# Optimization experiments

Hardware: AMD Instinct MI355X
Metric: run time of the kernel (lower is better)

## Reference

```python
import jax, jax.numpy as jnp
import numpy as np

B = 262144
VD = 64          # vector_dim
N_ACTION = 8     # n_orientation + n_position
N_TYPE = 5
IN_DIM = 6 + N_ACTION  # (n_orientation + n_bounding_box) + n_action = 14


def _linear_init(k, fan_in, fan_out):
    k1, k2 = jax.random.split(k)
    s = 1.0 / np.sqrt(fan_in)
    W = jax.random.uniform(k1, (fan_in, fan_out), minval=-s, maxval=s, dtype=jnp.float32)
    b = jax.random.uniform(k2, (fan_out,), minval=-s, maxval=s, dtype=jnp.float32)
    return W, b


def setup_inputs() -> dict:
    key = jax.random.key(0)
    ks = jax.random.split(key, 12)
    W1, b1 = _linear_init(ks[0], IN_DIM, VD)
    W1b, b1b = _linear_init(ks[1], VD, VD)
    W1c, b1c = _linear_init(ks[2], VD, VD)
    W2a, b2a = _linear_init(ks[3], VD, N_ACTION)
    W2b, b2b = _linear_init(ks[4], VD, 1)
    Ta1, ta1 = _linear_init(ks[5], N_TYPE, VD)
    Ta2, ta2 = _linear_init(ks[6], VD, VD)
    Tb1, tb1 = _linear_init(ks[7], N_TYPE, VD)
    Tb2, tb2 = _linear_init(ks[8], VD, VD)
    states = jax.random.normal(ks[9], (B, 3, 18), dtype=jnp.float32)
    action = jax.random.normal(ks[10], (B, N_ACTION), dtype=jnp.float32)
    b_type = jax.random.normal(ks[11], (B, N_TYPE), dtype=jnp.float32)
    table = jnp.zeros((B, 6), dtype=jnp.float32)
    return dict(states=states, action=action, b_type=b_type, table=table,
                W1=W1, b1=b1, W1b=W1b, b1b=b1b, W1c=W1c, b1c=b1c,
                W2a=W2a, b2a=b2a, W2b=W2b, b2b=b2b,
                Ta1=Ta1, ta1=ta1, Ta2=Ta2, ta2=ta2,
                Tb1=Tb1, tb1=tb1, Tb2=Tb2, tb2=tb2)


def reference(states, action, b_type, table,
              W1, b1, W1b, b1b, W1c, b1c, W2a, b2a, W2b, b2b,
              Ta1, ta1, Ta2, ta2, Tb1, tb1, Tb2, tb2):
    def type_mlp(t, Wx, bx, Wy, by):  # Linear -> Tanh -> Linear -> Tanh
        return jnp.tanh(jnp.tanh(t @ Wx + bx) @ Wy + by)

    gate1 = type_mlp(b_type, Ta1, ta1, Ta2, ta2)  # [B, VD], type_a(b_type)

    # relative_positions: repeat action over n_blocks+1 slots, subtract block xy from first 3
    rel = jnp.tile(action[:, None, :], (1, 4, 1))          # [B, 4, 8]
    rel = rel.at[:, :3, :2].add(-states[:, :, :2])

    types = states[..., 13:18]                             # [B, 3, 5]
    st = states[..., 3:9]                                  # orientation+bbox slice, [B, 3, 6]

    def stack(x, g1):  # tanh(l1) -> tanh(l1b) -> *type_1 -> tanh(l1c)
        h = jnp.tanh(x @ W1 + b1)
        h = jnp.tanh(h @ W1b + b1b) * g1
        return jnp.tanh(h @ W1c + b1c)

    # table branch (no second type gating)
    h_t = stack(jnp.concatenate([rel[:, 3], table], axis=-1), gate1)  # [B, VD]
    w_t = jax.nn.sigmoid(h_t @ W2b + b2b)                             # [B, 1]
    v_t = h_t @ W2a + b2a                                             # [B, 8]

    # three neighbor branches, vectorized over the block axis
    xin = jnp.concatenate([rel[:, :3], st], axis=-1)       # [B, 3, 14]
    h = stack(xin, gate1[:, None, :])                      # [B, 3, VD]
    h = h * type_mlp(types, Tb1, tb1, Tb2, tb2)            # gate by type_b(types[:, i])
    w = jax.nn.sigmoid(h @ W2b + b2b)                      # [B, 3, 1]
    v = h @ W2a + b2a                                      # [B, 3, 8]

    mask = st[:, :, 0:1] != -1.0                           # [B, 3, 1]
    w = jnp.where(mask, w, 0.0)

    residuals = w_t * v_t + jnp.sum(w * v, axis=1)         # [B, 8]
    return residuals + action
```

## Files before the change

### kernel.cpp

```cpp
#include <hip/hip_runtime.h>

typedef unsigned int  uint;
typedef unsigned short u16;
typedef __attribute__((ext_vector_type(8))) short bf16x8;
typedef __attribute__((ext_vector_type(4))) float f32x4;

#define OF_W1B   0
#define OF_W1C   4096
#define OF_TA2   8192
#define OF_TB2   12288
#define SHW_U16  16384
#define OF_W1    16384
#define OF_TA1   18432
#define OF_TB1   20480
#define OF_W2AB  22528
#define WTOT     23552
#define BTA2 0
#define BTB2 64
#define BB1B 128
#define BB1C 192
#define BH   256
#define BIASN 272

#if defined(__has_builtin) && __has_builtin(__builtin_amdgcn_exp2f)
#define EXP2F(x) __builtin_amdgcn_exp2f(x)
#else
#define EXP2F(x) __expf((x) * 0.6931471805599453f)
#endif
#if defined(__has_builtin) && __has_builtin(__builtin_amdgcn_rcpf)
#define RCPF(x) __builtin_amdgcn_rcpf(x)
#else
#define RCPF(x) __fdividef(1.0f, (x))
#endif

__device__ __forceinline__ float ftanh(float x){
    const float e = EXP2F(x * 2.8853900817779268f);
    return __builtin_fmaf(-2.0f, RCPF(e + 1.0f), 1.0f);
}
__device__ __forceinline__ float fsigm(float x){
    return RCPF(1.0f + EXP2F(-1.4426950408889634f * x));
}
__device__ __forceinline__ uint cvtpk(float lo, float hi){
    uint r; asm("v_cvt_pk_bf16_f32 %0, %1, %2" : "=v"(r) : "v"(lo), "v"(hi)); return r;
}
__device__ __forceinline__ u16 bfb(float x){
    union { float f; uint u; } v; v.f = x;
    return (u16)((v.u + 0x7fffu + ((v.u >> 16) & 1u)) >> 16);
}
__device__ __forceinline__ f32x4 MFMA(bf16x8 a, bf16x8 b, f32x4 c){
    return __builtin_amdgcn_mfma_f32_16x16x32_bf16(a, b, c, 0, 0, 0);
}

__device__ __forceinline__ void zacc(f32x4 (&acc)[4][2]){
    #pragma unroll
    for (int mt = 0; mt < 4; ++mt)
        #pragma unroll
        for (int n = 0; n < 2; ++n) acc[mt][n] = f32x4{0.f, 0.f, 0.f, 0.f};
}
__device__ __forceinline__ void ld_bias(const float* SB, int bb, int q, f32x4 (&acc)[4][2]){
    #pragma unroll
    for (int mt = 0; mt < 4; ++mt){
        const f32x4 b4 = *(const f32x4*)&SB[bb + 16*mt + 4*q];
        acc[mt][0] = b4; acc[mt][1] = b4;
    }
}

__device__ __forceinline__ void layer_k32(const u16* __restrict__ AbG, const u16* Bb, int WB,
                                          f32x4 (&acc)[4][2]){
    bf16x8 A[4];
    #pragma unroll
    for (int mt = 0; mt < 4; ++mt) A[mt] = *(const bf16x8*)&AbG[WB + mt*512];
    #pragma unroll
    for (int n = 0; n < 2; ++n){
        const bf16x8 B = *(const bf16x8*)&Bb[n*1024];
        #pragma unroll
        for (int mt = 0; mt < 4; ++mt) acc[mt][n] = MFMA(A[mt], B, acc[mt][n]);
    }
}
__device__ __forceinline__ void layer_k64(const u16* AbL, const u16* Bb, int WB,
                                          f32x4 (&acc)[4][2]){
    #pragma unroll
    for (int s = 0; s < 2; ++s){
        bf16x8 A[4];
        #pragma unroll
        for (int mt = 0; mt < 4; ++mt) A[mt] = *(const bf16x8*)&AbL[WB + (mt*2+s)*512];
        #pragma unroll
        for (int n = 0; n < 2; ++n){
            const bf16x8 B = *(const bf16x8*)&Bb[n*1024 + s*512];
            #pragma unroll
            for (int mt = 0; mt < 4; ++mt) acc[mt][n] = MFMA(A[mt], B, acc[mt][n]);
        }
    }
}
__device__ __forceinline__ void head_k64(const u16* __restrict__ AbG, const u16* Bb,
                                         f32x4 (&ah)[2]){
    const bf16x8 A0 = *(const bf16x8*)&AbG[OF_W2AB];
    const bf16x8 A1 = *(const bf16x8*)&AbG[OF_W2AB + 512];
    #pragma unroll
    for (int n = 0; n < 2; ++n){
        const bf16x8 B0 = *(const bf16x8*)&Bb[n*1024];
        const bf16x8 B1 = *(const bf16x8*)&Bb[n*1024 + 512];
        ah[n] = MFMA(A0, B0, ah[n]);
        ah[n] = MFMA(A1, B1, ah[n]);
    }
}

__device__ __forceinline__ void stD(u16* EW, int mt, int n, uint lo, uint hi){
    *(uint2*)&EW[(n*2 + (mt>>1))*512 + (mt&1)*256] = make_uint2(lo, hi);
}
__device__ __forceinline__ void epi_tanh(u16* EW, const f32x4 (&acc)[4][2]){
    #pragma unroll
    for (int mt = 0; mt < 4; ++mt)
        #pragma unroll
        for (int n = 0; n < 2; ++n)
            stD(EW, mt, n, cvtpk(ftanh(acc[mt][n][0]), ftanh(acc[mt][n][1])),
                           cvtpk(ftanh(acc[mt][n][2]), ftanh(acc[mt][n][3])));
}

template<int NR>
__device__ __forceinline__ void write_xrow(u16* ACW, int lane, const float (&x)[NR]){
    uint buf[16];
    #pragma unroll
    for (int i = 0; i < 16; ++i){
        if (2*i < NR){
            const float lo = x[2*i];
            const float hi = (2*i+1 < NR) ? x[2*i+1] : 0.f;
            buf[i] = cvtpk(lo, hi);
        } else buf[i] = 0u;
    }
    buf[15] = 0x3F800000u;
    const int c = lane & 31, n = c >> 4, col = c & 15, h = lane >> 5;
    #pragma unroll
    for (int gg = 0; gg < 2; ++gg){
        const int g = 2*h + gg;
        *(uint4*)&ACW[n*1024 + (g*16 + col)*8] =
            make_uint4(buf[4*g], buf[4*g+1], buf[4*g+2], buf[4*g+3]);
    }
}

__global__ __launch_bounds__(256)
void prep_weights(const float* __restrict__ W1,  const float* __restrict__ b1,
                  const float* __restrict__ W1b, const float* __restrict__ b1b,
                  const float* __restrict__ W1c, const float* __restrict__ b1c,
                  const float* __restrict__ W2a, const float* __restrict__ b2a,
                  const float* __restrict__ W2b, const float* __restrict__ b2b,
                  const float* __restrict__ Ta1, const float* __restrict__ ta1,
                  const float* __restrict__ Ta2, const float* __restrict__ ta2,
                  const float* __restrict__ Tb1, const float* __restrict__ tb1,
                  const float* __restrict__ Tb2, const float* __restrict__ tb2,
                  u16* __restrict__ WS)
{
    const int b = blockIdx.x, tid = threadIdx.x;
    if (b < 4){
        const float* Wg = (b==0) ? W1b : (b==1) ? W1c : (b==2) ? Ta2 : Tb2;
        const int    bb = (b==0) ? OF_W1B : (b==1) ? OF_W1C : (b==2) ? OF_TA2 : OF_TB2;
        #pragma unroll 1
        for (int idx = tid; idx < 4096; idx += 256){
            const int k = idx >> 6, j = idx & 63;
            WS[bb + (((j>>4)<<1)|(k>>5))*512 + ((j&15)|(((k>>3)&3)<<4))*8 + (k&7)] = bfb(Wg[idx]);
        }
        return;
    }
    float* WB = (float*)(WS + WTOT);
    #pragma unroll 1
    for (int i = tid; i < (WTOT - OF_W1); i += 256) WS[OF_W1 + i] = 0;
    __syncthreads();
    #pragma unroll 1
    for (int idx = tid; idx < 896; idx += 256){
        const int k = idx >> 6, j = idx & 63;
        WS[OF_W1 + (j>>4)*512 + ((j&15)|(((k>>3)&3)<<4))*8 + (k&7)] = bfb(W1[idx]);
    }
    #pragma unroll 1
    for (int idx = tid; idx < 320; idx += 256){
        const int k = idx >> 6, j = idx & 63;
        const int d = (j>>4)*512 + ((j&15)|(((k>>3)&3)<<4))*8 + (k&7);
        WS[OF_TA1 + d] = bfb(Ta1[idx]);
        WS[OF_TB1 + d] = bfb(Tb1[idx]);
    }
    #pragma unroll 1
    for (int idx = tid; idx < 512; idx += 256){
        const int j = idx >> 3, i = idx & 7;
        WS[OF_W2AB + (j>>5)*512 + (i|(((j>>3)&3)<<4))*8 + (j&7)] = bfb(W2a[idx]);
    }
    if (tid < 64){
        const int j = tid;
        WS[OF_W2AB + (j>>5)*512 + (8|(((j>>3)&3)<<4))*8 + (j&7)] = bfb(W2b[j]);
        const int d31 = ((j&15)|(3<<4))*8 + 7;
        WS[OF_W1  + (j>>4)*512 + d31] = bfb(b1[j]);
        WS[OF_TA1 + (j>>4)*512 + d31] = bfb(ta1[j]);
        WS[OF_TB1 + (j>>4)*512 + d31] = bfb(tb1[j]);
        WB[BTA2+j] = ta2[j]; WB[BTB2+j] = tb2[j];
        WB[BB1B+j] = b1b[j]; WB[BB1C+j] = b1c[j];
    }
    if (tid < 16) WB[BH+tid] = (tid < 8) ? b2a[tid] : (tid == 8 ? b2b[0] : 0.0f);
}

__global__ __launch_bounds__(256)
__attribute__((amdgpu_waves_per_eu(3, 3)))
void net_mfma(const float* __restrict__ states, const float* __restrict__ action,
              const float* __restrict__ b_type, const float* __restrict__ table,
              const u16* __restrict__ WS, int Btot, float* __restrict__ out)
{
    __shared__ u16   SHW[SHW_U16];
    __shared__ float SBIAS[BIASN];
    __shared__ u16   ACT[4*2048];

    const int tid  = threadIdx.x;
    const int lane = tid & 63;
    const int q    = lane >> 4;
    const int wv   = tid >> 6;

    {
        const uint4* src = (const uint4*)WS;
        uint4* dst = (uint4*)SHW;
        #pragma unroll 1
        for (int i = tid; i < SHW_U16/8; i += 256) dst[i] = src[i];
        const float* bg = (const float*)(WS + WTOT);
        #pragma unroll 1
        for (int i = tid; i < BIASN; i += 256) SBIAS[i] = bg[i];
    }
    __syncthreads();

    u16* ACW = &ACT[wv << 11];
    const u16* AbG = &WS[lane*8];
    const u16* AbL = &SHW[lane*8];
    const u16* Bb  = &ACW[lane*8];
    u16* EW = &ACW[(q>>1)*128 + (lane&15)*8 + 4*(q&1)];

    const int ebw   = blockIdx.x*128 + wv*32;
    const int elast = Btot - 1;
    const int eme   = min(ebw + (lane & 31), elast);

    float a8[8];
    { const float* ap = action + (size_t)eme*8;
      const float4 a0 = *(const float4*)ap; const float4 a1 = *(const float4*)(ap+4);
      a8[0]=a0.x; a8[1]=a0.y; a8[2]=a0.z; a8[3]=a0.w; a8[4]=a1.x; a8[5]=a1.y; a8[6]=a1.z; a8[7]=a1.w; }
    const float* sp = states + (size_t)eme*54;

    uint2 gp[4][2];
    {
        float x5[5];
        { const float* bp = b_type + (size_t)eme*5;
          #pragma unroll
          for (int k = 0; k < 5; ++k) x5[k] = bp[k]; }
        write_xrow<5>(ACW, lane, x5);
        f32x4 acc[4][2];
        zacc(acc);
        layer_k32(AbG, Bb, OF_TA1, acc);
        epi_tanh(EW, acc);
        ld_bias(SBIAS, BTA2, q, acc);
        layer_k64(AbL, Bb, OF_TA2, acc);
        #pragma unroll
        for (int mt = 0; mt < 4; ++mt)
            #pragma unroll
            for (int n = 0; n < 2; ++n)
                gp[mt][n] = make_uint2(cvtpk(ftanh(acc[mt][n][0]), ftanh(acc[mt][n][1])),
                                       cvtpk(ftanh(acc[mt][n][2]), ftanh(acc[mt][n][3])));
    }

    f32x4 ro[2];
    ro[0] = f32x4{0.f,0.f,0.f,0.f}; ro[1] = f32x4{0.f,0.f,0.f,0.f};

    #pragma unroll 1
    for (int r = 0; r < 4; ++r){
        const bool ht = (r < 3);
        uint2 tgp[4][2];
        f32x4 acc[4][2];

        if (ht){
            float xt[5];
            #pragma unroll
            for (int k = 0; k < 5; ++k) xt[k] = sp[r*18 + 13 + k];
            write_xrow<5>(ACW, lane, xt);
            zacc(acc);
            layer_k32(AbG, Bb, OF_TB1, acc);
            epi_tanh(EW, acc);
            ld_bias(SBIAS, BTB2, q, acc);
            layer_k64(AbL, Bb, OF_TB2, acc);
            #pragma unroll
            for (int mt = 0; mt < 4; ++mt)
                #pragma unroll
                for (int n = 0; n < 2; ++n)
                    tgp[mt][n] = make_uint2(cvtpk(ftanh(acc[mt][n][0]), ftanh(acc[mt][n][1])),
                                            cvtpk(ftanh(acc[mt][n][2]), ftanh(acc[mt][n][3])));
        }

        float x14[14]; float maskf = 1.0f;
        #pragma unroll
        for (int k = 0; k < 8; ++k) x14[k] = a8[k];
        if (ht){
            x14[0] -= sp[r*18 + 0];
            x14[1] -= sp[r*18 + 1];
            #pragma unroll
            for (int k = 0; k < 6; ++k) x14[8 + k] = sp[r*18 + 3 + k];
            maskf = (x14[8] == -1.0f) ? 0.0f : 1.0f;
        } else {
            const float* tp = table + (size_t)eme*6;
            #pragma unroll
            for (int k = 0; k < 6; ++k) x14[8 + k] = tp[k];
        }
        write_xrow<14>(ACW, lane, x14);

        zacc(acc);
        layer_k32(AbG, Bb, OF_W1, acc);
        epi_tanh(EW, acc);

        ld_bias(SBIAS, BB1B, q, acc);
        layer_k64(AbL, Bb, OF_W1B, acc);
        #pragma unroll
        for (int mt = 0; mt < 4; ++mt)
            #pragma unroll
            for (int n = 0; n < 2; ++n){
                const uint lo = gp[mt][n].x, hi = gp[mt][n].y;
                const float t0 = ftanh(acc[mt][n][0]) * __uint_as_float(lo << 16);
                const float t1 = ftanh(acc[mt][n][1]) * __uint_as_float(lo & 0xffff0000u);
                const float t2 = ftanh(acc[mt][n][2]) * __uint_as_float(hi << 16);
                const float t3 = ftanh(acc[mt][n][3]) * __uint_as_float(hi & 0xffff0000u);
                stD(EW, mt, n, cvtpk(t0, t1), cvtpk(t2, t3));
            }

        ld_bias(SBIAS, BB1C, q, acc);
        layer_k64(AbL, Bb, OF_W1C, acc);
        #pragma unroll
        for (int mt = 0; mt < 4; ++mt)
            #pragma unroll
            for (int n = 0; n < 2; ++n){
                float m0 = 1.f, m1 = 1.f, m2 = 1.f, m3 = 1.f;
                if (ht){
                    const uint lo = tgp[mt][n].x, hi = tgp[mt][n].y;
                    m0 = __uint_as_float(lo << 16); m1 = __uint_as_float(lo & 0xffff0000u);
                    m2 = __uint_as_float(hi << 16); m3 = __uint_as_float(hi & 0xffff0000u);
                }
                stD(EW, mt, n, cvtpk(ftanh(acc[mt][n][0])*m0, ftanh(acc[mt][n][1])*m1),
                               cvtpk(ftanh(acc[mt][n][2])*m2, ftanh(acc[mt][n][3])*m3));
            }

        f32x4 ah[2];
        { const f32x4 b4 = *(const f32x4*)&SBIAS[BH + 4*q];
          ah[0] = b4; ah[1] = b4; }
        head_k64(AbG, Bb, ah);

        #pragma unroll
        for (int n = 0; n < 2; ++n){
            const float wm = fsigm(ah[n][0]);
            const float w  = __shfl(wm, 32 + (lane & 15), 64)
                           * __shfl(maskf, 16*n + (lane & 15), 64);
            #pragma unroll
            for (int c = 0; c < 4; ++c) ro[n][c] += w * ah[n][c];
        }
    }

    if (lane < 32){
        #pragma unroll
        for (int n = 0; n < 2; ++n){
            const int e2 = ebw + 16*n + (lane & 15);
            if (e2 < Btot){
                const int co = 4*q;
                const float4 av = *(const float4*)(action + (size_t)e2*8 + co);
                float4 res;
                res.x = av.x + ro[n][0]; res.y = av.y + ro[n][1];
                res.z = av.z + ro[n][2]; res.w = av.w + ro[n][3];
                *(float4*)(out + (size_t)e2*8 + co) = res;
            }
        }
    }
}

extern "C" void kernel_launch(void* const* d_in, const int* in_sizes, int n_in,
                              void* d_out, int out_size, void* d_ws, size_t ws_size,
                              hipStream_t stream)
{
    const float* states = (const float*)d_in[0];
    const float* action = (const float*)d_in[1];
    const float* b_type = (const float*)d_in[2];
    const float* table  = (const float*)d_in[3];
    const float* W1  = (const float*)d_in[4];
    const float* b1  = (const float*)d_in[5];
    const float* W1b = (const float*)d_in[6];
    const float* b1b = (const float*)d_in[7];
    const float* W1c = (const float*)d_in[8];
    const float* b1c = (const float*)d_in[9];
    const float* W2a = (const float*)d_in[10];
    const float* b2a = (const float*)d_in[11];
    const float* W2b = (const float*)d_in[12];
    const float* b2b = (const float*)d_in[13];
    const float* Ta1 = (const float*)d_in[14];
    const float* ta1 = (const float*)d_in[15];
    const float* Ta2 = (const float*)d_in[16];
    const float* ta2 = (const float*)d_in[17];
    const float* Tb1 = (const float*)d_in[18];
    const float* tb1 = (const float*)d_in[19];
    const float* Tb2 = (const float*)d_in[20];
    const float* tb2 = (const float*)d_in[21];
    float* out = (float*)d_out;
    u16* WS = (u16*)d_ws;

    const int Btot = in_sizes[1] / 8;
    prep_weights<<<dim3(5), dim3(256), 0, stream>>>(
        W1, b1, W1b, b1b, W1c, b1c, W2a, b2a, W2b, b2b,
        Ta1, ta1, Ta2, ta2, Tb1, tb1, Tb2, tb2, WS);
    const int grid = (Btot + 127) / 128;
    net_mfma<<<dim3(grid), dim3(256), 0, stream>>>(
        states, action, b_type, table, WS, Btot, out);
}
```

Measured before the change: 142.9 us.

## Split MFMA layers per N-tile and double block size to raise occupancy

Each layer now runs over the two 16-column N tiles one at a time, with sched_barrier fences between them, so only four accumulator tiles are live at once instead of eight. Weight A-fragments are loaded inside the MFMA loop rather than preloaded. The block grows to 512 threads (8 waves, 256 elements) with waves_per_eu relaxed to 3-4, so the shared-memory weight copy is amortised over more elements and occupancy can rise. The cost is repeated A-fragment loads for each N tile, and the fences limit how much the compiler can overlap MFMA with the tanh epilogue.

```diff
diff --git a/kernel.cpp b/kernel.cpp
--- a/kernel.cpp
+++ b/kernel.cpp
@@ -32,6 +32,7 @@
 #else
 #define RCPF(x) __fdividef(1.0f, (x))
 #endif
+#define SCHED_FENCE() __builtin_amdgcn_sched_barrier(0)
 
 __device__ __forceinline__ float ftanh(float x){
     const float e = EXP2F(x * 2.8853900817779268f);
@@ -51,70 +52,56 @@
     return __builtin_amdgcn_mfma_f32_16x16x32_bf16(a, b, c, 0, 0, 0);
 }
 
-__device__ __forceinline__ void zacc(f32x4 (&acc)[4][2]){
+__device__ __forceinline__ void zacc4(f32x4 (&acc)[4]){
+    #pragma unroll
+    for (int mt = 0; mt < 4; ++mt) acc[mt] = f32x4{0.f, 0.f, 0.f, 0.f};
+}
+__device__ __forceinline__ void ldb4(const float* SB, int bb, int q, f32x4 (&acc)[4]){
     #pragma unroll
     for (int mt = 0; mt < 4; ++mt)
-        #pragma unroll
-        for (int n = 0; n < 2; ++n) acc[mt][n] = f32x4{0.f, 0.f, 0.f, 0.f};
-}
-__device__ __forceinline__ void ld_bias(const float* SB, int bb, int q, f32x4 (&acc)[4][2]){
+        acc[mt] = *(const f32x4*)&SB[bb + 16*mt + 4*q];
+}
+
+__device__ __forceinline__ void k32_n(const u16* __restrict__ Ab, const u16* Bb, int WB,
+                                      int n, f32x4 (&acc)[4]){
+    const bf16x8 B = *(const bf16x8*)&Bb[n*1024];
     #pragma unroll
     for (int mt = 0; mt < 4; ++mt){
-        const f32x4 b4 = *(const f32x4*)&SB[bb + 16*mt + 4*q];
-        acc[mt][0] = b4; acc[mt][1] = b4;
-    }
-}
-
-__device__ __forceinline__ void layer_k32(const u16* __restrict__ AbG, const u16* Bb, int WB,
-                                          f32x4 (&acc)[4][2]){
-    bf16x8 A[4];
-    #pragma unroll
-    for (int mt = 0; mt < 4; ++mt) A[mt] = *(const bf16x8*)&AbG[WB + mt*512];
-    #pragma unroll
-    for (int n = 0; n < 2; ++n){
-        const bf16x8 B = *(const bf16x8*)&Bb[n*1024];
-        #pragma unroll
-        for (int mt = 0; mt < 4; ++mt) acc[mt][n] = MFMA(A[mt], B, acc[mt][n]);
-    }
-}
-__device__ __forceinline__ void layer_k64(const u16* AbL, const u16* Bb, int WB,
-                                          f32x4 (&acc)[4][2]){
+        const bf16x8 A = *(const bf16x8*)&Ab[WB + mt*512];
+        acc[mt] = MFMA(A, B, acc[mt]);
+    }
+}
+__device__ __forceinline__ void k64_n(const u16* AbL, const u16* Bb, int WB,
+                                      int n, f32x4 (&acc)[4]){
     #pragma unroll
     for (int s = 0; s < 2; ++s){
-        bf16x8 A[4];
-        #pragma unroll
-        for (int mt = 0; mt < 4; ++mt) A[mt] = *(const bf16x8*)&AbL[WB + (mt*2+s)*512];
-        #pragma unroll
-        for (int n = 0; n < 2; ++n){
-            const bf16x8 B = *(const bf16x8*)&Bb[n*1024 + s*512];
-            #pragma unroll
-            for (int mt = 0; mt < 4; ++mt) acc[mt][n] = MFMA(A[mt], B, acc[mt][n]);
-        }
-    }
-}
-__device__ __forceinline__ void head_k64(const u16* __restrict__ AbG, const u16* Bb,
-                                         f32x4 (&ah)[2]){
-    const bf16x8 A0 = *(const bf16x8*)&AbG[OF_W2AB];
-    const bf16x8 A1 = *(const bf16x8*)&AbG[OF_W2AB + 512];
-    #pragma unroll
-    for (int n = 0; n < 2; ++n){
-        const bf16x8 B0 = *(const bf16x8*)&Bb[n*1024];
-        const bf16x8 B1 = *(const bf16x8*)&Bb[n*1024 + 512];
-        ah[n] = MFMA(A0, B0, ah[n]);
-        ah[n] = MFMA(A1, B1, ah[n]);
-    }
+        const bf16x8 B = *(const bf16x8*)&Bb[n*1024 + s*512];
+        #pragma unroll
+        for (int mt = 0; mt < 4; ++mt){
+            const bf16x8 A = *(const bf16x8*)&AbL[WB + (mt*2+s)*512];
+            acc[mt] = MFMA(A, B, acc[mt]);
+        }
+    }
+}
+__device__ __forceinline__ f32x4 head_n(const u16* __restrict__ Ab, const u16* Bb,
+                                        int n, f32x4 ah){
+    #pragma unroll
+    for (int s = 0; s < 2; ++s){
+        const bf16x8 A = *(const bf16x8*)&Ab[OF_W2AB + s*512];
+        const bf16x8 B = *(const bf16x8*)&Bb[n*1024 + s*512];
+        ah = MFMA(A, B, ah);
+    }
+    return ah;
 }
 
 __device__ __forceinline__ void stD(u16* EW, int mt, int n, uint lo, uint hi){
     *(uint2*)&EW[(n*2 + (mt>>1))*512 + (mt&1)*256] = make_uint2(lo, hi);
 }
-__device__ __forceinline__ void epi_tanh(u16* EW, const f32x4 (&acc)[4][2]){
+__device__ __forceinline__ void epi_tanh_n(u16* EW, int n, const f32x4 (&acc)[4]){
     #pragma unroll
     for (int mt = 0; mt < 4; ++mt)
-        #pragma unroll
-        for (int n = 0; n < 2; ++n)
-            stD(EW, mt, n, cvtpk(ftanh(acc[mt][n][0]), ftanh(acc[mt][n][1])),
-                           cvtpk(ftanh(acc[mt][n][2]), ftanh(acc[mt][n][3])));
+        stD(EW, mt, n, cvtpk(ftanh(acc[mt][0]), ftanh(acc[mt][1])),
+                       cvtpk(ftanh(acc[mt][2]), ftanh(acc[mt][3])));
 }
 
 template<int NR>
@@ -195,15 +182,15 @@
     if (tid < 16) WB[BH+tid] = (tid < 8) ? b2a[tid] : (tid == 8 ? b2b[0] : 0.0f);
 }
 
-__global__ __launch_bounds__(256)
-__attribute__((amdgpu_waves_per_eu(3, 3)))
+__global__ __launch_bounds__(512)
+__attribute__((amdgpu_waves_per_eu(3, 4)))
 void net_mfma(const float* __restrict__ states, const float* __restrict__ action,
               const float* __restrict__ b_type, const float* __restrict__ table,
               const u16* __restrict__ WS, int Btot, float* __restrict__ out)
 {
     __shared__ u16   SHW[SHW_U16];
     __shared__ float SBIAS[BIASN];
-    __shared__ u16   ACT[4*2048];
+    __shared__ u16   ACT[8*2048];
 
     const int tid  = threadIdx.x;
     const int lane = tid & 63;
@@ -214,10 +201,9 @@
         const uint4* src = (const uint4*)WS;
         uint4* dst = (uint4*)SHW;
         #pragma unroll 1
-        for (int i = tid; i < SHW_U16/8; i += 256) dst[i] = src[i];
+        for (int i = tid; i < SHW_U16/8; i += 512) dst[i] = src[i];
         const float* bg = (const float*)(WS + WTOT);
-        #pragma unroll 1
-        for (int i = tid; i < BIASN; i += 256) SBIAS[i] = bg[i];
+        if (tid < BIASN) SBIAS[tid] = bg[tid];
     }
     __syncthreads();
 
@@ -227,7 +213,7 @@
     const u16* Bb  = &ACW[lane*8];
     u16* EW = &ACW[(q>>1)*128 + (lane&15)*8 + 4*(q&1)];
 
-    const int ebw   = blockIdx.x*128 + wv*32;
+    const int ebw   = blockIdx.x*256 + wv*32;
     const int elast = Btot - 1;
     const int eme   = min(ebw + (lane & 31), elast);
 
@@ -244,18 +230,20 @@
           #pragma unroll
           for (int k = 0; k < 5; ++k) x5[k] = bp[k]; }
         write_xrow<5>(ACW, lane, x5);
-        f32x4 acc[4][2];
-        zacc(acc);
-        layer_k32(AbG, Bb, OF_TA1, acc);
-        epi_tanh(EW, acc);
-        ld_bias(SBIAS, BTA2, q, acc);
-        layer_k64(AbL, Bb, OF_TA2, acc);
-        #pragma unroll
-        for (int mt = 0; mt < 4; ++mt)
-            #pragma unroll
-            for (int n = 0; n < 2; ++n)
-                gp[mt][n] = make_uint2(cvtpk(ftanh(acc[mt][n][0]), ftanh(acc[mt][n][1])),
-                                       cvtpk(ftanh(acc[mt][n][2]), ftanh(acc[mt][n][3])));
+        #pragma unroll
+        for (int n = 0; n < 2; ++n){
+            f32x4 acc[4];
+            zacc4(acc);
+            k32_n(AbG, Bb, OF_TA1, n, acc);
+            epi_tanh_n(EW, n, acc);
+            ldb4(SBIAS, BTA2, q, acc);
+            k64_n(AbL, Bb, OF_TA2, n, acc);
+            #pragma unroll
+            for (int mt = 0; mt < 4; ++mt)
+                gp[mt][n] = make_uint2(cvtpk(ftanh(acc[mt][0]), ftanh(acc[mt][1])),
+                                       cvtpk(ftanh(acc[mt][2]), ftanh(acc[mt][3])));
+            SCHED_FENCE();
+        }
     }
 
     f32x4 ro[2];
@@ -265,24 +253,26 @@
     for (int r = 0; r < 4; ++r){
         const bool ht = (r < 3);
         uint2 tgp[4][2];
-        f32x4 acc[4][2];
 
         if (ht){
             float xt[5];
             #pragma unroll
             for (int k = 0; k < 5; ++k) xt[k] = sp[r*18 + 13 + k];
             write_xrow<5>(ACW, lane, xt);
-            zacc(acc);
-            layer_k32(AbG, Bb, OF_TB1, acc);
-            epi_tanh(EW, acc);
-            ld_bias(SBIAS, BTB2, q, acc);
-            layer_k64(AbL, Bb, OF_TB2, acc);
-            #pragma unroll
-            for (int mt = 0; mt < 4; ++mt)
+            #pragma unroll
+            for (int n = 0; n < 2; ++n){
+                f32x4 acc[4];
+                zacc4(acc);
+                k32_n(AbG, Bb, OF_TB1, n, acc);
+                epi_tanh_n(EW, n, acc);
+                ldb4(SBIAS, BTB2, q, acc);
+                k64_n(AbL, Bb, OF_TB2, n, acc);
                 #pragma unroll
-                for (int n = 0; n < 2; ++n)
-                    tgp[mt][n] = make_uint2(cvtpk(ftanh(acc[mt][n][0]), ftanh(acc[mt][n][1])),
-                                            cvtpk(ftanh(acc[mt][n][2]), ftanh(acc[mt][n][3])));
+                for (int mt = 0; mt < 4; ++mt)
+                    tgp[mt][n] = make_uint2(cvtpk(ftanh(acc[mt][0]), ftanh(acc[mt][1])),
+                                            cvtpk(ftanh(acc[mt][2]), ftanh(acc[mt][3])));
+                SCHED_FENCE();
+            }
         }
 
         float x14[14]; float maskf = 1.0f;
@@ -301,52 +291,61 @@
         }
         write_xrow<14>(ACW, lane, x14);
 
-        zacc(acc);
-        layer_k32(AbG, Bb, OF_W1, acc);
-        epi_tanh(EW, acc);
-
-        ld_bias(SBIAS, BB1B, q, acc);
-        layer_k64(AbL, Bb, OF_W1B, acc);
-        #pragma unroll
-        for (int mt = 0; mt < 4; ++mt)
-            #pragma unroll
-            for (int n = 0; n < 2; ++n){
+        #pragma unroll
+        for (int n = 0; n < 2; ++n){
+            f32x4 acc[4];
+            zacc4(acc);
+            k32_n(AbG, Bb, OF_W1, n, acc);
+            epi_tanh_n(EW, n, acc);
+            SCHED_FENCE();
+        }
+
+        #pragma unroll
+        for (int n = 0; n < 2; ++n){
+            f32x4 acc[4];
+            ldb4(SBIAS, BB1B, q, acc);
+            k64_n(AbL, Bb, OF_W1B, n, acc);
+            #pragma unroll
+            for (int mt = 0; mt < 4; ++mt){
                 const uint lo = gp[mt][n].x, hi = gp[mt][n].y;
-                const float t0 = ftanh(acc[mt][n][0]) * __uint_as_float(lo << 16);
-                const float t1 = ftanh(acc[mt][n][1]) * __uint_as_float(lo & 0xffff0000u);
-                const float t2 = ftanh(acc[mt][n][2]) * __uint_as_float(hi << 16);
-                const float t3 = ftanh(acc[mt][n][3]) * __uint_as_float(hi & 0xffff0000u);
+                const float t0 = ftanh(acc[mt][0]) * __uint_as_float(lo << 16);
+                const float t1 = ftanh(acc[mt][1]) * __uint_as_float(lo & 0xffff0000u);
+                const float t2 = ftanh(acc[mt][2]) * __uint_as_float(hi << 16);
+                const float t3 = ftanh(acc[mt][3]) * __uint_as_float(hi & 0xffff0000u);
                 stD(EW, mt, n, cvtpk(t0, t1), cvtpk(t2, t3));
             }
-
-        ld_bias(SBIAS, BB1C, q, acc);
-        layer_k64(AbL, Bb, OF_W1C, acc);
-        #pragma unroll
-        for (int mt = 0; mt < 4; ++mt)
-            #pragma unroll
-            for (int n = 0; n < 2; ++n){
+            SCHED_FENCE();
+        }
+
+        #pragma unroll
+        for (int n = 0; n < 2; ++n){
+            f32x4 acc[4];
+            ldb4(SBIAS, BB1C, q, acc);
+            k64_n(AbL, Bb, OF_W1C, n, acc);
+            #pragma unroll
+            for (int mt = 0; mt < 4; ++mt){
                 float m0 = 1.f, m1 = 1.f, m2 = 1.f, m3 = 1.f;
                 if (ht){
                     const uint lo = tgp[mt][n].x, hi = tgp[mt][n].y;
                     m0 = __uint_as_float(lo << 16); m1 = __uint_as_float(lo & 0xffff0000u);
                     m2 = __uint_as_float(hi << 16); m3 = __uint_as_float(hi & 0xffff0000u);
                 }
-                stD(EW, mt, n, cvtpk(ftanh(acc[mt][n][0])*m0, ftanh(acc[mt][n][1])*m1),
-                               cvtpk(ftanh(acc[mt][n][2])*m2, ftanh(acc[mt][n][3])*m3));
+                stD(EW, mt, n, cvtpk(ftanh(acc[mt][0])*m0, ftanh(acc[mt][1])*m1),
+                               cvtpk(ftanh(acc[mt][2])*m2, ftanh(acc[mt][3])*m3));
             }
-
-        f32x4 ah[2];
-        { const f32x4 b4 = *(const f32x4*)&SBIAS[BH + 4*q];
-          ah[0] = b4; ah[1] = b4; }
-        head_k64(AbG, Bb, ah);
-
-        #pragma unroll
-        for (int n = 0; n < 2; ++n){
-            const float wm = fsigm(ah[n][0]);
+            SCHED_FENCE();
+        }
+
+        #pragma unroll
+        for (int n = 0; n < 2; ++n){
+            f32x4 ah = *(const f32x4*)&SBIAS[BH + 4*q];
+            ah = head_n(AbG, Bb, n, ah);
+            const float wm = fsigm(ah[0]);
             const float w  = __shfl(wm, 32 + (lane & 15), 64)
                            * __shfl(maskf, 16*n + (lane & 15), 64);
             #pragma unroll
-            for (int c = 0; c < 4; ++c) ro[n][c] += w * ah[n][c];
+            for (int c = 0; c < 4; ++c) ro[n][c] += w * ah[c];
+            SCHED_FENCE();
         }
     }
 
@@ -399,7 +398,7 @@
     prep_weights<<<dim3(5), dim3(256), 0, stream>>>(
         W1, b1, W1b, b1b, W1c, b1c, W2a, b2a, W2b, b2b,
         Ta1, ta1, Ta2, ta2, Tb1, tb1, Tb2, tb2, WS);
-    const int grid = (Btot + 127) / 128;
-    net_mfma<<<dim3(grid), dim3(256), 0, stream>>>(
+    const int grid = (Btot + 255) / 256;
+    net_mfma<<<dim3(grid), dim3(512), 0, stream>>>(
         states, action, b_type, table, WS, Btot, out);
 }
```

New measurement: 149.8 us. 1.05x slower.
